# Kernel tuning notes

Measured on AMD Instinct MI355X. Metric: run time of the kernel, lower is better.

Reference implementation:

```python
import jax, jax.numpy as jnp
import numpy as np

EPS = 1e-5
DN = ('NCHW', 'OIHW', 'NCHW')

def conv3(x, w):
    return jax.lax.conv_general_dilated(x, w, (1, 1), 'SAME', dimension_numbers=DN)

def conv1(x, w, b):
    # w: [O, I]
    return jnp.einsum('oi,bihw->bohw', w, x) + b[None, :, None, None]

def bn_relu(x, p):
    # p: [4, C] rows = scale, bias, mean, var (eval-mode BatchNorm2d)
    s, b, m, v = p[0], p[1], p[2], p[3]
    y = s[None, :, None, None] * (x - m[None, :, None, None]) * jax.lax.rsqrt(v[None, :, None, None] + EPS) + b[None, :, None, None]
    return jax.nn.relu(y)

def setup_inputs() -> dict:
    key = jax.random.key(0)
    ks = jax.random.split(key, 24)
    B, Cin, H, W = 2, 2048, 60, 60
    Ci = Cin // 4            # 512 inter_channels
    Cq = Ci // 8             # 64  query/key channels
    Co = 40                  # out_channels (classes)
    f32 = jnp.float32
    def bn(C):
        return jnp.stack([jnp.ones((C,), f32), jnp.zeros((C,), f32), jnp.zeros((C,), f32), jnp.ones((C,), f32)])
    s3 = 1.0 / np.sqrt(9 * Ci)
    inp = {
        'x': jax.random.normal(ks[0], (B, Cin, H, W), f32),
        'd': jax.random.uniform(ks[1], (B, 1, H, W), f32),
        'w_s0': jax.random.normal(ks[2], (Ci, Cin, 3, 3), f32) * (1.0 / np.sqrt(9 * Cin)),
        'bn_s0': bn(Ci),
        'wq': jax.random.normal(ks[3], (Cq, Ci), f32) * (1.0 / np.sqrt(Ci)),
        'bq': jnp.zeros((Cq,), f32),
        'wk': jax.random.normal(ks[4], (Cq, Ci), f32) * (1.0 / np.sqrt(Ci)),
        'bk': jnp.zeros((Cq,), f32),
        'wv': jax.random.normal(ks[5], (Ci, Ci), f32) * (1.0 / np.sqrt(Ci)),
        'bv': jnp.zeros((Ci,), f32),
        'gamma_sa': jnp.zeros((), f32) + 0.5,   # nonzero so attention branch contributes
        'lamb': jnp.zeros((), f32) + 0.3,
        'w_s1': jax.random.normal(ks[6], (Ci, Ci, 3, 3), f32) * s3,
        'bn_s1': bn(Ci),
        'w6': jax.random.normal(ks[7], (Co, Ci), f32) * (1.0 / np.sqrt(Ci)),
        'b6': jnp.zeros((Co,), f32),
        'w_c0': jax.random.normal(ks[8], (Ci, Cin, 3, 3), f32) * (1.0 / np.sqrt(9 * Cin)),
        'bn_c0': bn(Ci),
        'gamma_sc': jnp.zeros((), f32) + 0.5,
        'w_c1': jax.random.normal(ks[9], (Ci, Ci, 3, 3), f32) * s3,
        'bn_c1': bn(Ci),
        'w7': jax.random.normal(ks[10], (Co, Ci), f32) * (1.0 / np.sqrt(Ci)),
        'b7': jnp.zeros((Co,), f32),
        'w8': jax.random.normal(ks[11], (Co, Ci), f32) * (1.0 / np.sqrt(Ci)),
        'b8': jnp.zeros((Co,), f32),
    }
    return inp

def reference(x, d, w_s0, bn_s0, wq, bq, wk, bk, wv, bv, gamma_sa, lamb,
              w_s1, bn_s1, w6, b6, w_c0, bn_c0, gamma_sc, w_c1, bn_c1, w7, b7, w8, b8):
    B, _, H, W = x.shape
    N = H * W
    # ---- position-attention (PAM_Module_Dep, fuse_type='a', depth_order=2) branch ----
    feat1 = bn_relu(conv3(x, w_s0), bn_s0)               # [B, Ci, H, W]
    Ci = feat1.shape[1]
    q = conv1(feat1, wq, bq).reshape(B, -1, N)           # [B, Cq, N]
    k = conv1(feat1, wk, bk).reshape(B, -1, N)           # [B, Cq, N]
    v = conv1(feat1, wv, bv).reshape(B, Ci, N)           # [B, Ci, N]
    energy = jnp.einsum('bcn,bcm->bnm', q, k)            # [B, N, N], n=query pixel
    df = d.reshape(B, N)
    dd = (df[:, :, None] - df[:, None, :]) ** 2          # depth_order == 2
    attention = jax.nn.softmax(energy + lamb * dd, axis=-1)
    sa = jnp.einsum('bcm,bnm->bcn', v, attention).reshape(B, Ci, H, W)
    sa = gamma_sa * sa + feat1
    sa_conv = bn_relu(conv3(sa, w_s1), bn_s1)            # post_conv=True
    sa_output = conv1(sa_conv, w6, b6)                   # Dropout2d is identity in eval
    # ---- channel-attention (CAM_Module) branch ----
    feat2 = bn_relu(conv3(x, w_c0), bn_c0)               # [B, Ci, H, W]
    xf = feat2.reshape(B, Ci, N)
    cen = jnp.einsum('bcn,bdn->bcd', xf, xf)             # [B, Ci, Ci]
    cen = jnp.max(cen, axis=-1, keepdims=True) - cen
    catt = jax.nn.softmax(cen, axis=-1)
    sc = jnp.einsum('bcd,bdn->bcn', catt, xf).reshape(B, Ci, H, W)
    sc = gamma_sc * sc + feat2
    sc_conv = bn_relu(conv3(sc, w_c1), bn_c1)
    sc_output = conv1(sc_conv, w7, b7)
    # ---- fusion head ----
    feat_sum = sa_conv + sc_conv
    sasc_output = conv1(feat_sum, w8, b8)
    return (sasc_output, sa_output, sc_output)
```

## Files before the change

kernel.cpp:

```cpp
#include <hip/hip_runtime.h>
#include <stdint.h>

#define DI __device__ __forceinline__

typedef unsigned short u16;
typedef unsigned int u32;
typedef __attribute__((ext_vector_type(8))) short short8;
typedef __attribute__((ext_vector_type(4))) float floatx4;

constexpr int NPIX = 3600;
constexpr int NK   = 3712;
constexpr int PP   = 4096;
constexpr int GUARD= 128;
constexpr int CIN  = 2048, CI = 512, CQ = 64;

constexpr size_t OFF_XPM    = 0;
constexpr size_t OFF_SAF    = 0;
constexpr size_t OFF_PBUF   = 14745600;
constexpr size_t OFF_SACONV = 0;
constexpr size_t OFF_SCCONV = 8388608;
constexpr size_t R1_END     = 42812416;
constexpr size_t OFF_FEAT1  = R1_END;
constexpr size_t OFF_FEAT2  = OFF_FEAT1 + 8388608;
constexpr size_t OFF_SAPM   = OFF_FEAT2 + 8388608;
constexpr size_t OFF_SCPM   = OFF_SAPM + 8912896;
constexpr size_t OFF_W      = OFF_SCPM + 8912896;
constexpr size_t OFF_WQB = OFF_W;
constexpr size_t OFF_QC  = OFF_W + 655360;
constexpr size_t OFF_KC  = OFF_W + 1576960;
constexpr size_t OFF_VC  = OFF_W + 2498560;
constexpr size_t OFF_WT1 = OFF_W;
constexpr size_t OFF_WT2 = OFF_W + 4718592;
constexpr size_t OFF_VCM = OFF_W + 9871360;
constexpr size_t OFF_CEN = OFF_W + 17473536;
constexpr size_t OFF_CATT= OFF_W + 19570688;
constexpr size_t OFF_WH  = OFF_W + 20619264;
constexpr size_t WS_NEED = OFF_W + 37748736;

DI float b2f(u16 s){ u32 u = ((u32)s)<<16; float f; __builtin_memcpy(&f,&u,4); return f; }
DI u16 f2b(float f){ u32 u; __builtin_memcpy(&u,&f,4); u32 r=(u+0x7fffu+((u>>16)&1u))>>16; return (u16)r; }
DI int pad_of(int n){ int y=n/60, x=n-y*60; return ((y+2)<<6)+x+2; }
DI bool interior(int p){ int py=p>>6, px=p&63; return (py>=2)&&(py<62)&&(px>=2)&&(px<62); }
DI int compact_of(int p){ return ((p>>6)-2)*60 + (p&63) - 2; }
DI void gll16(const void* g, void* l){
  __builtin_amdgcn_global_load_lds((const __attribute__((address_space(1))) void*)g,
                                   (__attribute__((address_space(3))) void*)l, 16, 0, 0);
}
DI float wred_min(float v){
#pragma unroll
  for(int m=32;m;m>>=1) v=fminf(v,__shfl_xor(v,m,64));
  return v;
}
DI float wred_sum(float v){
#pragma unroll
  for(int m=32;m;m>>=1) v+=__shfl_xor(v,m,64);
  return v;
}

struct GArgs {
  const u16 *A, *A2, *B, *B2; u16 *Cb, *Cb2, *Cb3; float* Cf;
  const u16* resid;
  const float *bn, *bn2, *bias, *bias2, *bias3, *gamma, *lambp, *dR, *dC;
  long sA, sB, sC, sres;
  int M, N, KT, ktps, lda, ldb, ldc, Mclamp, Nclamp, nsplit, ksplit, kps;
};

template<int MODE, bool SHIFT, bool NCAT, bool DUALZ, int U, bool SPLITK, bool KCAT2=false>
__global__ __launch_bounds__(256) void k_gemm(GArgs g){
  __shared__ alignas(16) short As[U*4096];
  __shared__ alignas(16) short Bs[U*4096];
  const int bz = blockIdx.z;
  const int sel = DUALZ ? (bz>>1) : 0;
  int bt  = DUALZ ? (bz&1)  : bz;
  int slice = 0;
  if constexpr(SPLITK){ bt = bz / g.ksplit; slice = bz - bt*g.ksplit; }
  const u16* Ab = ((DUALZ && sel) ? g.A2 : g.A) + (long)bt*g.sA;
  const u16* Ab2 = KCAT2 ? (g.A2 + (long)bt*g.sA) : nullptr;
  const u16* Bb = ((DUALZ && sel) ? g.B2 : g.B) + (long)bt*g.sB;
  const int m0 = blockIdx.x*128, n0 = blockIdx.y*128;
  const int tid = threadIdx.x, wid = tid>>6, lane = tid&63;
  const int wr = wid>>1, wc = wid&1;
  const int fr = lane&15, fq = lane>>4;
  const int srow = lane>>2;
  const int swz = ((lane&3) ^ ((lane>>3)&3)) << 3;

  long raB[2], rbB[2];
#pragma unroll
  for(int h=0;h<2;h++){
    long ra = m0 + wid*32 + h*16 + srow;
    if (!SHIFT) ra = (ra > g.Mclamp) ? (long)g.Mclamp : ra;
    raB[h] = ra*(long)g.lda + swz;
    long rb = n0 + wid*32 + h*16 + srow;
    rb = (rb > g.Nclamp) ? (long)g.Nclamp : rb;
    rbB[h] = rb*(long)g.ldb + swz;
  }
  const int ldsOff[2] = { (wid*32)*64, (wid*32+16)*64 };
  const int rswz = (fq ^ ((fr>>1)&3)) << 3;
  const int aRdO = (wr*64+fr)*32 + rswz;
  const int bRdO = (wc*64+fr)*32 + rswz;

  floatx4 acc[4][4];
#pragma unroll
  for(int i=0;i<4;i++)
#pragma unroll
    for(int j=0;j<4;j++)
#pragma unroll
      for(int e=0;e<4;e++) acc[i][j][e]=0.f;

  if constexpr(SHIFT){
    const int KB = g.ktps;
    for(int s=0; s<9; ++s){
      const long aoff = (long)((s/3)*64 + (s-(s/3)*3) - 65)*g.lda;
      const long boff = (long)s*KB*32;
      for(int kb=0; kb<KB; kb+=U){
        __syncthreads();
#pragma unroll
        for(int u=0;u<U;++u){
          const int ko = (kb+u)*32;
#pragma unroll
          for(int h=0;h<2;h++){
            gll16(Ab + raB[h] + aoff + ko, (char*)As + u*8192 + ldsOff[h]);
            gll16(Bb + rbB[h] + boff + ko, (char*)Bs + u*8192 + ldsOff[h]);
          }
        }
        __syncthreads();
#pragma unroll
        for(int u=0;u<U;++u){
          short8 af[4], bfv[4];
#pragma unroll
          for(int mi=0;mi<4;mi++) af[mi]  = *(const short8*)(As + u*4096 + aRdO + mi*512);
#pragma unroll
          for(int ni=0;ni<4;ni++) bfv[ni] = *(const short8*)(Bs + u*4096 + bRdO + ni*512);
#pragma unroll
          for(int mi=0;mi<4;mi++)
#pragma unroll
            for(int ni=0;ni<4;ni++)
              acc[mi][ni] = __builtin_amdgcn_mfma_f32_16x16x32_bf16(af[mi], bfv[ni], acc[mi][ni], 0,0,0);
        }
      }
    }
  } else {
    int kt0 = 0, ktN = g.KT;
    if constexpr(SPLITK){ kt0 = slice*g.kps; ktN = min(g.KT, kt0+g.kps); }
    for(int kt=kt0; kt<ktN; kt+=U){
      __syncthreads();
#pragma unroll
      for(int u=0;u<U;++u){
        if (kt+u < ktN){
          int ko = kt+u;
          const u16* srcA = Ab;
          if constexpr(KCAT2){ if (ko >= (g.KT>>1)){ srcA = Ab2; ko -= (g.KT>>1); } }
          const int koB = (kt+u)*32;
#pragma unroll
          for(int h=0;h<2;h++){
            gll16(srcA + raB[h] + ko*32, (char*)As + u*8192 + ldsOff[h]);
            gll16(Bb + rbB[h] + koB, (char*)Bs + u*8192 + ldsOff[h]);
          }
        }
      }
      __syncthreads();
#pragma unroll
      for(int u=0;u<U;++u){
        if (kt+u < ktN){
          short8 af[4], bfv[4];
#pragma unroll
          for(int mi=0;mi<4;mi++) af[mi]  = *(const short8*)(As + u*4096 + aRdO + mi*512);
#pragma unroll
          for(int ni=0;ni<4;ni++) bfv[ni] = *(const short8*)(Bs + u*4096 + bRdO + ni*512);
#pragma unroll
          for(int mi=0;mi<4;mi++)
#pragma unroll
            for(int ni=0;ni<4;ni++)
              acc[mi][ni] = __builtin_amdgcn_mfma_f32_16x16x32_bf16(af[mi], bfv[ni], acc[mi][ni], 0,0,0);
        }
      }
    }
  }

  float* Cf = (MODE==3) ? g.Cf + (long)bt*g.sC : nullptr;
  const u16* Rb = (MODE==5) ? g.resid + (long)bt*g.sres : nullptr;
  float gamv=0.f;
  if constexpr(MODE==5) gamv = *g.gamma;

#pragma unroll
  for(int ni=0;ni<4;ni++){
    const int gc = n0 + wc*64 + ni*16 + fr;
    if (gc >= g.N) continue;
    if constexpr(MODE==0){
      const float* bnP = g.bn; u16* CbP = g.Cb; int oc = gc;
      if constexpr(DUALZ){ if (sel){ bnP = g.bn2; CbP = g.Cb2; } }
      if constexpr(NCAT){ if (gc >= g.nsplit){ bnP = g.bn2; CbP = g.Cb2; oc = gc - g.nsplit; } }
      CbP += (long)bt*g.sC;
      const float s_=bnP[oc], bb=bnP[CI+oc], mm=bnP[2*CI+oc], vv=bnP[3*CI+oc];
      const float cA = s_*rsqrtf(vv+1e-5f), cB = bb - cA*mm;
#pragma unroll
      for(int mi=0;mi<4;mi++)
#pragma unroll
        for(int j=0;j<4;j++){
          const int gr = m0 + wr*64 + mi*16 + fq*4 + j;
          if (interior(gr)) CbP[(size_t)gr*g.ldc + oc] = f2b(fmaxf(cA*acc[mi][ni][j]+cB, 0.f));
        }
    } else if constexpr(MODE==6){
      u16* dst; int col, ld; float bs;
      if (gc < 64){ dst = g.Cb  + (long)bt*((long)NPIX*CQ); col=gc;     ld=CQ; bs=g.bias[gc]; }
      else if (gc < 128){ dst = g.Cb2 + (long)bt*((long)NPIX*CQ); col=gc-64; ld=CQ; bs=g.bias2[gc-64]; }
      else { dst = g.Cb3 + (long)bt*((long)NPIX*CI); col=gc-128; ld=CI; bs=g.bias3[gc-128]; }
#pragma unroll
      for(int mi=0;mi<4;mi++)
#pragma unroll
        for(int j=0;j<4;j++){
          const int gr = m0 + wr*64 + mi*16 + fq*4 + j;
          if (interior(gr)) dst[(size_t)compact_of(gr)*ld + col] = f2b(acc[mi][ni][j] + bs);
        }
    } else if constexpr(MODE==3){
#pragma unroll
      for(int mi=0;mi<4;mi++)
#pragma unroll
        for(int j=0;j<4;j++){
          const int gr = m0 + wr*64 + mi*16 + fq*4 + j;
          if (gr < g.M){
            if constexpr(SPLITK) atomicAdd(&Cf[(size_t)gr*g.ldc + gc], acc[mi][ni][j]);
            else Cf[(size_t)gr*g.ldc + gc] = acc[mi][ni][j];
          }
        }
    } else if constexpr(MODE==5){
      u16* CbP = g.Cb + (long)bt*g.sC;
#pragma unroll
      for(int mi=0;mi<4;mi++)
#pragma unroll
        for(int j=0;j<4;j++){
          const int gr = m0 + wr*64 + mi*16 + fq*4 + j;
          if (interior(gr)){ const size_t o=(size_t)gr*g.ldc + gc; CbP[o] = f2b(gamv*acc[mi][ni][j] + b2f(Rb[o])); }
        }
    } else if constexpr(MODE==7){
      size_t hb; int oc; const float* bp;
      if (gc < 40){ hb = 0; oc = gc; bp = g.bias; }
      else if (gc < 80){ hb = 288000; oc = gc-40; bp = g.bias2; }
      else { hb = 576000; oc = gc-80; bp = g.bias3; }
      float* dst = g.Cf + hb + (size_t)bt*144000 + (size_t)oc*3600;
      const float bsv = bp[oc];
#pragma unroll
      for(int mi=0;mi<4;mi++)
#pragma unroll
        for(int j=0;j<4;j++){
          const int gr = m0 + wr*64 + mi*16 + fq*4 + j;
          if (interior(gr)) dst[compact_of(gr)] = acc[mi][ni][j] + bsv;
        }
    }
  }
}

__global__ __launch_bounds__(512) void k_esm(const u16* __restrict__ qc, const u16* __restrict__ kc,
    const float* __restrict__ dd, const float* __restrict__ lamp, u16* __restrict__ pb){
  __shared__ float lm[8][16], ll[8][16];
  const int tid = threadIdx.x, wave = tid>>6, lane = tid&63;
  const int fr = lane&15, fq = lane>>4;
  const int q0 = blockIdx.x*16;
  const float lam = *lamp;
  const u16* qp = qc + (size_t)(q0+fr)*CQ + fq*8;
  const short8 qa0 = *(const short8*)(qp);
  const short8 qa1 = *(const short8*)(qp + 32);
  float dr[4];
#pragma unroll
  for(int j=0;j<4;j++) dr[j] = dd[q0 + fq*4 + j];
  float m[4], l[4];
#pragma unroll
  for(int j=0;j<4;j++){ m[j] = -3e38f; l[j] = 0.f; }

  for(int t=wave; t<29; t+=8){
    const int n0 = t*128;
    floatx4 s[8]; float dc[8];
#pragma unroll
    for(int ni=0; ni<8; ++ni){
      const int ccol = min(n0 + ni*16 + fr, NPIX-1);
      const u16* kp = kc + (size_t)ccol*CQ + fq*8;
      const short8 b0 = *(const short8*)(kp);
      const short8 b1 = *(const short8*)(kp + 32);
      floatx4 z = {0.f,0.f,0.f,0.f};
      z = __builtin_amdgcn_mfma_f32_16x16x32_bf16(qa0, b0, z, 0,0,0);
      s[ni] = __builtin_amdgcn_mfma_f32_16x16x32_bf16(qa1, b1, z, 0,0,0);
      dc[ni] = dd[ccol];
    }
#pragma unroll
    for(int j=0;j<4;j++){
      float vals[8]; float tmax = -3e38f;
#pragma unroll
      for(int ni=0;ni<8;ni++){
        const float td = dr[j] - dc[ni];
        float v = s[ni][j] + lam*td*td;
        if (n0 + ni*16 + fr >= NPIX) v = -3e38f;
        vals[ni] = v; tmax = fmaxf(tmax, v);
      }
      tmax = fmaxf(tmax, __shfl_xor(tmax,1,64));
      tmax = fmaxf(tmax, __shfl_xor(tmax,2,64));
      tmax = fmaxf(tmax, __shfl_xor(tmax,4,64));
      tmax = fmaxf(tmax, __shfl_xor(tmax,8,64));
      const float mn = fmaxf(m[j], tmax);
      float ts = 0.f;
#pragma unroll
      for(int ni=0;ni<8;ni++) ts += __expf(vals[ni]-mn);
      ts += __shfl_xor(ts,1,64);
      ts += __shfl_xor(ts,2,64);
      ts += __shfl_xor(ts,4,64);
      ts += __shfl_xor(ts,8,64);
      l[j] = l[j]*__expf(m[j]-mn) + ts;
      m[j] = mn;
    }
  }
  if (fr == 0){
#pragma unroll
    for(int j=0;j<4;j++){ lm[wave][fq*4+j] = m[j]; ll[wave][fq*4+j] = l[j]; }
  }
  __syncthreads();
  float M[4], L[4];
#pragma unroll
  for(int j=0;j<4;j++){
    const int row = fq*4 + j;
    float mm = lm[0][row];
#pragma unroll
    for(int w=1;w<8;w++) mm = fmaxf(mm, lm[w][row]);
    float ss = 0.f;
#pragma unroll
    for(int w=0;w<8;w++) ss += ll[w][row]*__expf(lm[w][row]-mm);
    M[j] = mm; L[j] = 1.f/ss;
  }

  for(int t=wave; t<29; t+=8){
    const int n0 = t*128;
#pragma unroll
    for(int ni=0; ni<8; ++ni){
      const int col = n0 + ni*16 + fr;
      const int ccol = min(col, NPIX-1);
      const u16* kp = kc + (size_t)ccol*CQ + fq*8;
      const short8 b0 = *(const short8*)(kp);
      const short8 b1 = *(const short8*)(kp + 32);
      floatx4 z = {0.f,0.f,0.f,0.f};
      z = __builtin_amdgcn_mfma_f32_16x16x32_bf16(qa0, b0, z, 0,0,0);
      const floatx4 sv = __builtin_amdgcn_mfma_f32_16x16x32_bf16(qa1, b1, z, 0,0,0);
      const float dcv = dd[ccol];
#pragma unroll
      for(int j=0;j<4;j++){
        const int q = q0 + fq*4 + j;
        const float td = dr[j] - dcv;
        float v = sv[j] + lam*td*td;
        if (col >= NPIX) v = -3e38f;
        const float p = __expf(v - M[j])*L[j];
        pb[(size_t)q*NK + col] = f2b(p);
      }
    }
  }
}

__global__ __launch_bounds__(256) void k_zring(u16* __restrict__ base, int C, long slabStride){
  const int row = blockIdx.x, slab = blockIdx.y;
  bool z;
  if (row < GUARD || row >= GUARD+PP) z = true;
  else z = !interior(row - GUARD);
  if (!z) return;
  u16* p = base + (size_t)slab*slabStride + (size_t)row*C;
  for (int i = threadIdx.x*8; i < C; i += 256*8){
    uint4 zz = {0,0,0,0};
    *(uint4*)(p + i) = zz;
  }
}

__global__ __launch_bounds__(256) void k_padx(const float* __restrict__ x, u16* __restrict__ xpm){
  __shared__ alignas(16) u16 t[64][72];
  const int n0 = blockIdx.x*64, c0 = blockIdx.y*64, b = blockIdx.z;
  const float* xb = x + (size_t)b*CIN*NPIX;
  u16* ob = xpm + (size_t)b*(PP+2*GUARD)*CIN + (size_t)GUARD*CIN;
  const int tid = threadIdx.x;
#pragma unroll
  for(int pass=0; pass<2; ++pass){
    const int cl = pass*32 + (tid>>3);
    const int nn = (tid&7)*8;
    const int n = n0 + nn;
    const float* src = xb + (size_t)(c0+cl)*NPIX + n;
    u16 r[8];
    if (n + 7 < NPIX){
      const float4 v0 = *(const float4*)src;
      const float4 v1 = *(const float4*)(src+4);
      r[0]=f2b(v0.x); r[1]=f2b(v0.y); r[2]=f2b(v0.z); r[3]=f2b(v0.w);
      r[4]=f2b(v1.x); r[5]=f2b(v1.y); r[6]=f2b(v1.z); r[7]=f2b(v1.w);
    } else {
#pragma unroll
      for(int j=0;j<8;j++){ const int nj=n+j; r[j] = (nj<NPIX)? f2b(src[j]) : (u16)0; }
    }
    __builtin_memcpy(&t[cl][nn], r, 16);
  }
  __syncthreads();
#pragma unroll
  for(int pass=0; pass<2; ++pass){
    const int nl = pass*32 + (tid>>3);
    const int cc = (tid&7)*8;
    const int n = n0 + nl;
    if (n < NPIX){
      u16 v[8];
#pragma unroll
      for(int j=0;j<8;j++) v[j] = t[cc+j][nl];
      uint4 vv; __builtin_memcpy(&vv, v, 16);
      *(uint4*)(ob + (size_t)pad_of(n)*CIN + c0 + cc) = vv;
    }
  }
}

template<bool PADIN>
__global__ __launch_bounds__(256) void k_to_cm(const u16* __restrict__ in, u16* __restrict__ out,
                                               long sIn, long sOut){
  __shared__ alignas(16) u16 t[64][72];
  const int n0 = blockIdx.x*64, c0 = blockIdx.y*64, b = blockIdx.z;
  const u16* ib = in + (size_t)b*sIn;
  u16* ob = out + (size_t)b*sOut;
  const int tid = threadIdx.x;
#pragma unroll
  for(int pass=0; pass<2; ++pass){
    const int nl = pass*32 + (tid>>3);
    const int cc = (tid&7)*8;
    const int n = n0 + nl;
    uint4 v = {0,0,0,0};
    if (n < NPIX){
      const int r = PADIN ? pad_of(n) : n;
      v = *(const uint4*)(ib + (size_t)r*CI + c0 + cc);
    }
    *(uint4*)&t[nl][cc] = v;
  }
  __syncthreads();
#pragma unroll
  for(int pass=0; pass<2; ++pass){
    const int cl = pass*32 + (tid>>3);
    const int nn = (tid&7)*8;
    const int n = n0 + nn;
    if (n < NK){
      u16 v[8];
#pragma unroll
      for(int j=0;j<8;j++) v[j] = t[nn+j][cl];
      uint4 vv; __builtin_memcpy(&vv, v, 16);
      *(uint4*)(ob + (size_t)(c0+cl)*NK + n) = vv;
    }
  }
}

__global__ __launch_bounds__(256) void k_wt2(const float* __restrict__ wA, const float* __restrict__ wB,
                                             u16* __restrict__ wtA, u16* __restrict__ wtB, int Kc){
  const float* w = blockIdx.y ? wB : wA;
  u16* wt = blockIdx.y ? wtB : wtA;
  const int idx = blockIdx.x*256 + threadIdx.x;
  const int o = idx / Kc, i = idx - o*Kc;
  u16 v[9];
#pragma unroll
  for(int s=0;s<9;s++) v[s] = f2b(w[(size_t)idx*9 + s]);
#pragma unroll
  for(int s=0;s<9;s++) wt[(size_t)o*9*Kc + (size_t)s*Kc + i] = v[s];
}

__global__ __launch_bounds__(256) void k_cvt3(const float* __restrict__ a, int na,
                                              const float* __restrict__ b, int nb,
                                              const float* __restrict__ c, int nc,
                                              u16* __restrict__ dst){
  const int i = blockIdx.x*256 + threadIdx.x;
  float v;
  if (i < na) v = a[i];
  else if (i < na+nb) v = b[i-na];
  else if (i < na+nb+nc) v = c[i-na-nb];
  else return;
  dst[i] = f2b(v);
}

__global__ __launch_bounds__(256) void k_whead(const float* __restrict__ w6, const float* __restrict__ w7,
                                               const float* __restrict__ w8, u16* __restrict__ wh){
  const int idx = blockIdx.x*256 + threadIdx.x;
  const int r = idx >> 10, k = idx & 1023;
  float v = 0.f;
  if (r < 40) v = w8[r*512 + (k & 511)];
  else if (r < 80){ if (k < 512) v = w6[(r-40)*512 + k]; }
  else { if (k >= 512) v = w7[(r-80)*512 + (k-512)]; }
  wh[idx] = f2b(v);
}

__global__ __launch_bounds__(256) void k_csoftmax(const float* __restrict__ cen, u16* __restrict__ catt){
  const int c = blockIdx.x, b = blockIdx.y, tid = threadIdx.x;
  const float* e = cen + ((size_t)b*CI + c)*CI;
  u16* o = catt + ((size_t)b*CI + c)*CI;
  __shared__ float red[8];
  const float a0 = e[tid], a1 = e[tid+256];
  float lmin = fminf(a0,a1);
  lmin = wred_min(lmin);
  if((tid&63)==0) red[tid>>6]=lmin;
  __syncthreads();
  const float m0 = fminf(fminf(red[0],red[1]),fminf(red[2],red[3]));
  const float x0 = __expf(m0-a0), x1 = __expf(m0-a1);
  float ls = x0+x1;
  ls = wred_sum(ls);
  if((tid&63)==0) red[4+(tid>>6)]=ls;
  __syncthreads();
  const float inv = 1.f/(red[4]+red[5]+red[6]+red[7]);
  o[tid] = f2b(x0*inv); o[tid+256] = f2b(x1*inv);
}

__global__ __launch_bounds__(256) void k_pv_ep(const float* __restrict__ saf, const u16* __restrict__ f1,
                                               u16* __restrict__ sapm, const float* __restrict__ gamma){
  const int idx = blockIdx.x*256 + threadIdx.x;
  const int n = idx >> 6, c = (idx & 63) * 8;
  const float gam = *gamma;
  const int p = pad_of(n);
  const float4 v0 = *(const float4*)(saf + (size_t)n*CI + c);
  const float4 v1 = *(const float4*)(saf + (size_t)n*CI + c + 4);
  const uint4 rv = *(const uint4*)(f1 + (size_t)p*CI + c);
  const u16* rp = (const u16*)&rv;
  u16 o[8];
  o[0]=f2b(gam*v0.x + b2f(rp[0])); o[1]=f2b(gam*v0.y + b2f(rp[1]));
  o[2]=f2b(gam*v0.z + b2f(rp[2])); o[3]=f2b(gam*v0.w + b2f(rp[3]));
  o[4]=f2b(gam*v1.x + b2f(rp[4])); o[5]=f2b(gam*v1.y + b2f(rp[5]));
  o[6]=f2b(gam*v1.z + b2f(rp[6])); o[7]=f2b(gam*v1.w + b2f(rp[7]));
  uint4 ov; __builtin_memcpy(&ov, o, 16);
  *(uint4*)(sapm + (size_t)p*CI + c) = ov;
}

extern "C" void kernel_launch(void* const* d_in, const int* in_sizes, int n_in,
                              void* d_out, int out_size, void* d_ws, size_t ws_size,
                              hipStream_t stream){
  (void)in_sizes; (void)n_in; (void)out_size;
  if (ws_size < WS_NEED) return;

  const float* x    = (const float*)d_in[0];
  const float* dd   = (const float*)d_in[1];
  const float* w_s0 = (const float*)d_in[2];
  const float* bn_s0= (const float*)d_in[3];
  const float* wq   = (const float*)d_in[4];
  const float* bq   = (const float*)d_in[5];
  const float* wk   = (const float*)d_in[6];
  const float* bk   = (const float*)d_in[7];
  const float* wv   = (const float*)d_in[8];
  const float* bv   = (const float*)d_in[9];
  const float* gsa  = (const float*)d_in[10];
  const float* lam  = (const float*)d_in[11];
  const float* w_s1 = (const float*)d_in[12];
  const float* bn_s1= (const float*)d_in[13];
  const float* w6   = (const float*)d_in[14];
  const float* b6   = (const float*)d_in[15];
  const float* w_c0 = (const float*)d_in[16];
  const float* bn_c0= (const float*)d_in[17];
  const float* gsc  = (const float*)d_in[18];
  const float* w_c1 = (const float*)d_in[19];
  const float* bn_c1= (const float*)d_in[20];
  const float* w7   = (const float*)d_in[21];
  const float* b7   = (const float*)d_in[22];
  const float* w8   = (const float*)d_in[23];
  const float* b8   = (const float*)d_in[24];

  char* W = (char*)d_ws;
  u16*   XPM   = (u16*)(W + OFF_XPM);
  float* SAF   = (float*)(W + OFF_SAF);
  u16*   PB    = (u16*)(W + OFF_PBUF);
  u16*   SACONV= (u16*)(W + OFF_SACONV);
  u16*   SCCONV= (u16*)(W + OFF_SCCONV);
  u16*   F1    = (u16*)(W + OFF_FEAT1);
  u16*   F2    = (u16*)(W + OFF_FEAT2);
  u16*   SAPM  = (u16*)(W + OFF_SAPM);
  u16*   SCPM  = (u16*)(W + OFF_SCPM);
  u16*   WTT   = (u16*)(W + OFF_W);
  u16*   WQB   = (u16*)(W + OFF_WQB);
  u16*   QC    = (u16*)(W + OFF_QC);
  u16*   KC    = (u16*)(W + OFF_KC);
  u16*   VC    = (u16*)(W + OFF_VC);
  u16*   WT1   = (u16*)(W + OFF_WT1);
  u16*   WT2   = (u16*)(W + OFF_WT2);
  u16*   WH    = (u16*)(W + OFF_WH);
  u16*   VCM   = (u16*)(W + OFF_VCM);
  u16*   F2CM  = VCM;
  float* CEN   = (float*)(W + OFF_CEN);
  u16*   CATT  = (u16*)(W + OFF_CATT);
  float* OUT   = (float*)d_out;

  k_zring<<<dim3(PP+2*GUARD, 2),256,0,stream>>>(XPM,  CIN, (long)(PP+2*GUARD)*CIN);
  k_zring<<<dim3(PP+2*GUARD, 4),256,0,stream>>>(SAPM, CI,  (long)(PP+2*GUARD)*CI);

  k_padx<<<dim3(57,32,2),256,0,stream>>>(x, XPM);

  k_wt2<<<dim3((512*2048)/256, 2),256,0,stream>>>(w_s0, w_c0, WTT, WTT + (size_t)512*9*2048, 2048);
  GArgs a{};
  a.A = XPM + (size_t)GUARD*CIN; a.B = WTT; a.Cb = F1; a.Cb2 = F2;
  a.bn = bn_s0; a.bn2 = bn_c0;
  a.sA = (long)(PP+2*GUARD)*CIN; a.sB = 0; a.sC = (long)PP*CI;
  a.M = PP; a.N = 1024; a.nsplit = 512; a.KT = 576; a.ktps = 64;
  a.lda = CIN; a.ldb = 9*2048; a.ldc = CI; a.Mclamp = PP-1; a.Nclamp = 1023;
  k_gemm<0,true,true,false,4,false><<<dim3(32,8,2),256,0,stream>>>(a);

  k_cvt3<<<dim3((64*512+64*512+512*512)/256),256,0,stream>>>(wq, 64*512, wk, 64*512, wv, 512*512, WQB);

  GArgs q{};
  q.A = F1; q.sA = (long)PP*CI; q.lda = CI;
  q.M = PP; q.Mclamp = PP-1; q.KT = 16; q.ktps = 16;
  q.B = WQB; q.sB = 0; q.ldb = CI; q.N = 640; q.Nclamp = 639;
  q.Cb = QC; q.Cb2 = KC; q.Cb3 = VC; q.bias = bq; q.bias2 = bk; q.bias3 = bv;
  k_gemm<6,false,false,false,4,false><<<dim3(32,5,2),256,0,stream>>>(q);

  k_to_cm<false><<<dim3(NK/64, CI/64, 2),256,0,stream>>>(VC, VCM, (long)NPIX*CI, (long)CI*NK);

  for(int bb=0; bb<2; ++bb){
    k_esm<<<dim3(225),512,0,stream>>>(QC + (size_t)bb*NPIX*CQ, KC + (size_t)bb*NPIX*CQ,
                                      dd + (size_t)bb*NPIX, lam, PB);
    hipMemsetAsync(SAF, 0, (size_t)NPIX*CI*4, stream);
    GArgs p{};
    p.A = PB; p.B = VCM + (size_t)bb*CI*NK;
    p.Cf = SAF;
    p.M = NPIX; p.N = CI; p.KT = NK/32; p.ktps = NK/32;
    p.lda = NK; p.ldb = NK; p.ldc = CI; p.sC = 0;
    p.Mclamp = NPIX-1; p.Nclamp = CI-1;
    p.ksplit = 4; p.kps = NK/128;
    k_gemm<3,false,false,false,4,true><<<dim3(29, 4, 4),256,0,stream>>>(p);
    k_pv_ep<<<dim3(NPIX*CI/8/256),256,0,stream>>>(SAF, F1 + (size_t)bb*PP*CI,
                                                  SAPM + (size_t)bb*(PP+2*GUARD)*CI + (size_t)GUARD*CI, gsa);
  }

  k_to_cm<true><<<dim3(NK/64, CI/64, 2),256,0,stream>>>(F2, F2CM, (long)PP*CI, (long)CI*NK);
  hipMemsetAsync(CEN, 0, (size_t)2*CI*CI*4, stream);
  GArgs c{};
  c.A = F2CM; c.B = F2CM; c.Cf = CEN;
  c.sA = (long)CI*NK; c.sB = (long)CI*NK; c.sC = (long)CI*CI;
  c.M = CI; c.N = CI; c.KT = NK/32; c.ktps = NK/32;
  c.lda = NK; c.ldb = NK; c.ldc = CI; c.Mclamp = CI-1; c.Nclamp = CI-1;
  c.ksplit = 8; c.kps = (NK/32 + 7)/8;
  k_gemm<3,false,false,false,1,true><<<dim3(4, 4, 16),256,0,stream>>>(c);
  k_csoftmax<<<dim3(CI,2),256,0,stream>>>(CEN, CATT);
  GArgs s{};
  s.A = F2; s.B = CATT;
  s.Cb = SCPM + (size_t)GUARD*CI;
  s.resid = F2; s.gamma = gsc;
  s.sA = (long)PP*CI; s.sB = (long)CI*CI; s.sC = (long)(PP+2*GUARD)*CI; s.sres = (long)PP*CI;
  s.M = PP; s.N = CI; s.KT = 16; s.ktps = 16;
  s.lda = CI; s.ldb = CI; s.ldc = CI; s.Mclamp = PP-1; s.Nclamp = CI-1;
  k_gemm<5,false,false,false,4,false><<<dim3(32, 4, 2),256,0,stream>>>(s);

  k_wt2<<<dim3((512*512)/256, 2),256,0,stream>>>(w_s1, w_c1, WT1, WT2, 512);
  k_whead<<<dim3(120*1024/256),256,0,stream>>>(w6, w7, w8, WH);
  GArgs t{};
  t.A = SAPM + (size_t)GUARD*CI; t.A2 = SCPM + (size_t)GUARD*CI;
  t.B = WT1; t.B2 = WT2;
  t.Cb = SACONV; t.Cb2 = SCCONV; t.bn = bn_s1; t.bn2 = bn_c1;
  t.sA = (long)(PP+2*GUARD)*CI; t.sB = 0; t.sC = (long)PP*CI;
  t.M = PP; t.N = CI; t.KT = 144; t.ktps = 16;
  t.lda = CI; t.ldb = 9*512; t.ldc = CI; t.Mclamp = PP-1; t.Nclamp = CI-1;
  k_gemm<0,true,false,true,4,false><<<dim3(32,4,4),256,0,stream>>>(t);

  GArgs h{};
  h.A = SACONV; h.A2 = SCCONV; h.B = WH; h.Cf = OUT;
  h.bias = b8; h.bias2 = b6; h.bias3 = b7;
  h.sA = (long)PP*CI; h.sB = 0; h.sC = 0;
  h.M = PP; h.N = 120; h.KT = 32; h.ktps = 32;
  h.lda = CI; h.ldb = 1024; h.ldc = 0; h.Mclamp = PP-1; h.Nclamp = 119;
  k_gemm<7,false,false,false,4,false,true><<<dim3(32,1,2),256,0,stream>>>(h);
}
```

Baseline: 740.6 us.

## Split-K first 3x3 conv per batch, cache ESM scores, stage probability writes via LDS

New measurement: 867.5 us. 1.17x slower.

```diff
diff --git a/kernel.cpp b/kernel.cpp
--- a/kernel.cpp
+++ b/kernel.cpp
@@ -62,7 +62,7 @@
   const u16* resid;
   const float *bn, *bn2, *bias, *bias2, *bias3, *gamma, *lambp, *dR, *dC;
   long sA, sB, sC, sres;
-  int M, N, KT, ktps, lda, ldb, ldc, Mclamp, Nclamp, nsplit, ksplit, kps;
+  int M, N, KT, ktps, lda, ldb, ldc, Mclamp, Nclamp, nsplit, ksplit, kps, kblog;
 };
 
 template<int MODE, bool SHIFT, bool NCAT, bool DUALZ, int U, bool SPLITK, bool KCAT2=false>
@@ -107,7 +107,45 @@
 #pragma unroll
       for(int e=0;e<4;e++) acc[i][j][e]=0.f;
 
-  if constexpr(SHIFT){
+  if constexpr(SHIFT && SPLITK){
+    const int KBm1 = g.ktps - 1;
+    const int kt0 = slice*g.kps;
+    const int ktN = min(g.KT, kt0 + g.kps);
+    for(int kt=kt0; kt<ktN; kt+=U){
+      __syncthreads();
+#pragma unroll
+      for(int u=0;u<U;++u){
+        const int gu = kt+u;
+        if (gu < ktN){
+          const int s_ = gu >> g.kblog;
+          const int s3 = s_/3;
+          const long aoff = (long)(s3*64 + (s_-s3*3) - 65)*g.lda + ((long)(gu & KBm1)<<5);
+          const long boff = (long)gu<<5;
+#pragma unroll
+          for(int h=0;h<2;h++){
+            gll16(Ab + raB[h] + aoff, (char*)As + u*8192 + ldsOff[h]);
+            gll16(Bb + rbB[h] + boff, (char*)Bs + u*8192 + ldsOff[h]);
+          }
+        }
+      }
+      __syncthreads();
+#pragma unroll
+      for(int u=0;u<U;++u){
+        if (kt+u < ktN){
+          short8 af[4], bfv[4];
+#pragma unroll
+          for(int mi=0;mi<4;mi++) af[mi]  = *(const short8*)(As + u*4096 + aRdO + mi*512);
+#pragma unroll
+          for(int ni=0;ni<4;ni++) bfv[ni] = *(const short8*)(Bs + u*4096 + bRdO + ni*512);
+#pragma unroll
+          for(int mi=0;mi<4;mi++)
+#pragma unroll
+            for(int ni=0;ni<4;ni++)
+              acc[mi][ni] = __builtin_amdgcn_mfma_f32_16x16x32_bf16(af[mi], bfv[ni], acc[mi][ni], 0,0,0);
+        }
+      }
+    }
+  } else if constexpr(SHIFT){
     const int KB = g.ktps;
     for(int s=0; s<9; ++s){
       const long aoff = (long)((s/3)*64 + (s-(s/3)*3) - 65)*g.lda;
@@ -250,9 +288,35 @@
   }
 }
 
+__global__ __launch_bounds__(256) void k_bnrelu(const float* __restrict__ cacc,
+    const float* __restrict__ bn1, const float* __restrict__ bn2,
+    u16* __restrict__ f1, u16* __restrict__ f2){
+  const int idx = blockIdx.x*256 + threadIdx.x;
+  const int n = idx >> 7, c = (idx & 127) * 8;
+  const int p = pad_of(n);
+  const float4 v0 = *(const float4*)(cacc + (size_t)p*1024 + c);
+  const float4 v1 = *(const float4*)(cacc + (size_t)p*1024 + c + 4);
+  const bool second = c >= 512;
+  const float* bn = second ? bn2 : bn1;
+  u16* f = second ? f2 : f1;
+  const int oc = c & 511;
+  const float vv[8] = {v0.x,v0.y,v0.z,v0.w,v1.x,v1.y,v1.z,v1.w};
+  u16 o[8];
+#pragma unroll
+  for(int j=0;j<8;j++){
+    const int ocj = oc + j;
+    const float s = bn[ocj], b = bn[CI+ocj], m = bn[2*CI+ocj], var = bn[3*CI+ocj];
+    const float cA = s*rsqrtf(var+1e-5f);
+    o[j] = f2b(fmaxf(cA*(vv[j]-m)+b, 0.f));
+  }
+  uint4 ov; __builtin_memcpy(&ov, o, 16);
+  *(uint4*)(f + (size_t)p*CI + oc) = ov;
+}
+
 __global__ __launch_bounds__(512) void k_esm(const u16* __restrict__ qc, const u16* __restrict__ kc,
     const float* __restrict__ dd, const float* __restrict__ lamp, u16* __restrict__ pb){
   __shared__ float lm[8][16], ll[8][16];
+  __shared__ alignas(16) u16 pemit[8][16][128];
   const int tid = threadIdx.x, wave = tid>>6, lane = tid&63;
   const int fr = lane&15, fq = lane>>4;
   const int q0 = blockIdx.x*16;
@@ -266,45 +330,50 @@
   float m[4], l[4];
 #pragma unroll
   for(int j=0;j<4;j++){ m[j] = -3e38f; l[j] = 0.f; }
-
-  for(int t=wave; t<29; t+=8){
-    const int n0 = t*128;
-    floatx4 s[8]; float dc[8];
-#pragma unroll
-    for(int ni=0; ni<8; ++ni){
-      const int ccol = min(n0 + ni*16 + fr, NPIX-1);
-      const u16* kp = kc + (size_t)ccol*CQ + fq*8;
-      const short8 b0 = *(const short8*)(kp);
-      const short8 b1 = *(const short8*)(kp + 32);
-      floatx4 z = {0.f,0.f,0.f,0.f};
-      z = __builtin_amdgcn_mfma_f32_16x16x32_bf16(qa0, b0, z, 0,0,0);
-      s[ni] = __builtin_amdgcn_mfma_f32_16x16x32_bf16(qa1, b1, z, 0,0,0);
-      dc[ni] = dd[ccol];
-    }
-#pragma unroll
-    for(int j=0;j<4;j++){
-      float vals[8]; float tmax = -3e38f;
-#pragma unroll
-      for(int ni=0;ni<8;ni++){
-        const float td = dr[j] - dc[ni];
-        float v = s[ni][j] + lam*td*td;
-        if (n0 + ni*16 + fr >= NPIX) v = -3e38f;
-        vals[ni] = v; tmax = fmaxf(tmax, v);
+  float vals[4][8][4];
+
+#pragma unroll
+  for(int tt=0; tt<4; ++tt){
+    const int t = wave + tt*8;
+    if (t < 29){
+      const int n0 = t*128;
+      floatx4 s[8]; float dc[8];
+#pragma unroll
+      for(int ni=0; ni<8; ++ni){
+        const int ccol = min(n0 + ni*16 + fr, NPIX-1);
+        const u16* kp = kc + (size_t)ccol*CQ + fq*8;
+        const short8 b0 = *(const short8*)(kp);
+        const short8 b1 = *(const short8*)(kp + 32);
+        floatx4 z = {0.f,0.f,0.f,0.f};
+        z = __builtin_amdgcn_mfma_f32_16x16x32_bf16(qa0, b0, z, 0,0,0);
+        s[ni] = __builtin_amdgcn_mfma_f32_16x16x32_bf16(qa1, b1, z, 0,0,0);
+        dc[ni] = dd[ccol];
       }
-      tmax = fmaxf(tmax, __shfl_xor(tmax,1,64));
-      tmax = fmaxf(tmax, __shfl_xor(tmax,2,64));
-      tmax = fmaxf(tmax, __shfl_xor(tmax,4,64));
-      tmax = fmaxf(tmax, __shfl_xor(tmax,8,64));
-      const float mn = fmaxf(m[j], tmax);
-      float ts = 0.f;
-#pragma unroll
-      for(int ni=0;ni<8;ni++) ts += __expf(vals[ni]-mn);
-      ts += __shfl_xor(ts,1,64);
-      ts += __shfl_xor(ts,2,64);
-      ts += __shfl_xor(ts,4,64);
-      ts += __shfl_xor(ts,8,64);
-      l[j] = l[j]*__expf(m[j]-mn) + ts;
-      m[j] = mn;
+#pragma unroll
+      for(int j=0;j<4;j++){
+        float tmax = -3e38f;
+#pragma unroll
+        for(int ni=0;ni<8;ni++){
+          const float td = dr[j] - dc[ni];
+          float v = s[ni][j] + lam*td*td;
+          if (n0 + ni*16 + fr >= NPIX) v = -3e38f;
+          vals[tt][ni][j] = v; tmax = fmaxf(tmax, v);
+        }
+        tmax = fmaxf(tmax, __shfl_xor(tmax,1,64));
+        tmax = fmaxf(tmax, __shfl_xor(tmax,2,64));
+        tmax = fmaxf(tmax, __shfl_xor(tmax,4,64));
+        tmax = fmaxf(tmax, __shfl_xor(tmax,8,64));
+        const float mn = fmaxf(m[j], tmax);
+        float ts = 0.f;
+#pragma unroll
+        for(int ni=0;ni<8;ni++) ts += __expf(vals[tt][ni][j]-mn);
+        ts += __shfl_xor(ts,1,64);
+        ts += __shfl_xor(ts,2,64);
+        ts += __shfl_xor(ts,4,64);
+        ts += __shfl_xor(ts,8,64);
+        l[j] = l[j]*__expf(m[j]-mn) + ts;
+        m[j] = mn;
+      }
     }
   }
   if (fr == 0){
@@ -325,27 +394,23 @@
     M[j] = mm; L[j] = 1.f/ss;
   }
 
-  for(int t=wave; t<29; t+=8){
-    const int n0 = t*128;
-#pragma unroll
-    for(int ni=0; ni<8; ++ni){
-      const int col = n0 + ni*16 + fr;
-      const int ccol = min(col, NPIX-1);
-      const u16* kp = kc + (size_t)ccol*CQ + fq*8;
-      const short8 b0 = *(const short8*)(kp);
-      const short8 b1 = *(const short8*)(kp + 32);
-      floatx4 z = {0.f,0.f,0.f,0.f};
-      z = __builtin_amdgcn_mfma_f32_16x16x32_bf16(qa0, b0, z, 0,0,0);
-      const floatx4 sv = __builtin_amdgcn_mfma_f32_16x16x32_bf16(qa1, b1, z, 0,0,0);
-      const float dcv = dd[ccol];
-#pragma unroll
-      for(int j=0;j<4;j++){
-        const int q = q0 + fq*4 + j;
-        const float td = dr[j] - dcv;
-        float v = sv[j] + lam*td*td;
-        if (col >= NPIX) v = -3e38f;
-        const float p = __expf(v - M[j])*L[j];
-        pb[(size_t)q*NK + col] = f2b(p);
+#pragma unroll
+  for(int tt=0; tt<4; ++tt){
+    const int t = wave + tt*8;
+    if (t < 29){
+      const int n0 = t*128;
+#pragma unroll
+      for(int ni=0;ni<8;ni++)
+#pragma unroll
+        for(int j=0;j<4;j++)
+          pemit[wave][fq*4+j][ni*16+fr] = f2b(__expf(vals[tt][ni][j] - M[j])*L[j]);
+      asm volatile("s_waitcnt lgkmcnt(0)" ::: "memory");
+#pragma unroll
+      for(int it=0; it<4; ++it){
+        const int row = it*4 + fq;
+        const int c8 = fr*8;
+        uint4 v; __builtin_memcpy(&v, &pemit[wave][row][c8], 16);
+        *(uint4*)(pb + (size_t)(q0+row)*NK + n0 + c8) = v;
       }
     }
   }
@@ -558,6 +623,7 @@
   u16*   F2    = (u16*)(W + OFF_FEAT2);
   u16*   SAPM  = (u16*)(W + OFF_SAPM);
   u16*   SCPM  = (u16*)(W + OFF_SCPM);
+  float* CACC  = (float*)(W + OFF_SAPM);
   u16*   WTT   = (u16*)(W + OFF_W);
   u16*   WQB   = (u16*)(W + OFF_WQB);
   u16*   QC    = (u16*)(W + OFF_QC);
@@ -573,18 +639,24 @@
   float* OUT   = (float*)d_out;
 
   k_zring<<<dim3(PP+2*GUARD, 2),256,0,stream>>>(XPM,  CIN, (long)(PP+2*GUARD)*CIN);
-  k_zring<<<dim3(PP+2*GUARD, 4),256,0,stream>>>(SAPM, CI,  (long)(PP+2*GUARD)*CI);
 
   k_padx<<<dim3(57,32,2),256,0,stream>>>(x, XPM);
 
   k_wt2<<<dim3((512*2048)/256, 2),256,0,stream>>>(w_s0, w_c0, WTT, WTT + (size_t)512*9*2048, 2048);
-  GArgs a{};
-  a.A = XPM + (size_t)GUARD*CIN; a.B = WTT; a.Cb = F1; a.Cb2 = F2;
-  a.bn = bn_s0; a.bn2 = bn_c0;
-  a.sA = (long)(PP+2*GUARD)*CIN; a.sB = 0; a.sC = (long)PP*CI;
-  a.M = PP; a.N = 1024; a.nsplit = 512; a.KT = 576; a.ktps = 64;
-  a.lda = CIN; a.ldb = 9*2048; a.ldc = CI; a.Mclamp = PP-1; a.Nclamp = 1023;
-  k_gemm<0,true,true,false,4,false><<<dim3(32,8,2),256,0,stream>>>(a);
+  for(int bb=0; bb<2; ++bb){
+    hipMemsetAsync(CACC, 0, (size_t)PP*1024*4, stream);
+    GArgs a{};
+    a.A = XPM + (size_t)bb*(PP+2*GUARD)*CIN + (size_t)GUARD*CIN;
+    a.B = WTT; a.Cf = CACC;
+    a.sA = 0; a.sB = 0; a.sC = 0;
+    a.M = PP; a.N = 1024; a.KT = 576; a.ktps = 64; a.kblog = 6;
+    a.lda = CIN; a.ldb = 9*2048; a.ldc = 1024; a.Mclamp = PP-1; a.Nclamp = 1023;
+    a.ksplit = 4; a.kps = 144;
+    k_gemm<3,true,false,false,2,true><<<dim3(32,8,4),256,0,stream>>>(a);
+    k_bnrelu<<<dim3(460800/256),256,0,stream>>>(CACC, bn_s0, bn_c0,
+        F1 + (size_t)bb*PP*CI, F2 + (size_t)bb*PP*CI);
+  }
+  k_zring<<<dim3(PP+2*GUARD, 4),256,0,stream>>>(SAPM, CI, (long)(PP+2*GUARD)*CI);
 
   k_cvt3<<<dim3((64*512+64*512+512*512)/256),256,0,stream>>>(wq, 64*512, wk, 64*512, wv, 512*512, WQB);
 
@@ -621,7 +693,7 @@
   c.M = CI; c.N = CI; c.KT = NK/32; c.ktps = NK/32;
   c.lda = NK; c.ldb = NK; c.ldc = CI; c.Mclamp = CI-1; c.Nclamp = CI-1;
   c.ksplit = 8; c.kps = (NK/32 + 7)/8;
-  k_gemm<3,false,false,false,1,true><<<dim3(4, 4, 16),256,0,stream>>>(c);
+  k_gemm<3,false,false,false,4,true><<<dim3(4, 4, 16),256,0,stream>>>(c);
   k_csoftmax<<<dim3(CI,2),256,0,stream>>>(CEN, CATT);
   GArgs s{};
   s.A = F2; s.B = CATT;
```

## Cache attention logits in registers and stage P writes through LDS

Applied to the files above, without the earlier changes.

After: 727.3 us. Within noise of the previous version (-1.8%).

```diff
diff --git a/kernel.cpp b/kernel.cpp
--- a/kernel.cpp
+++ b/kernel.cpp
@@ -253,6 +253,7 @@
 __global__ __launch_bounds__(512) void k_esm(const u16* __restrict__ qc, const u16* __restrict__ kc,
     const float* __restrict__ dd, const float* __restrict__ lamp, u16* __restrict__ pb){
   __shared__ float lm[8][16], ll[8][16];
+  __shared__ alignas(16) u16 pemit[8][16][128];
   const int tid = threadIdx.x, wave = tid>>6, lane = tid&63;
   const int fr = lane&15, fq = lane>>4;
   const int q0 = blockIdx.x*16;
@@ -266,45 +267,50 @@
   float m[4], l[4];
 #pragma unroll
   for(int j=0;j<4;j++){ m[j] = -3e38f; l[j] = 0.f; }
-
-  for(int t=wave; t<29; t+=8){
-    const int n0 = t*128;
-    floatx4 s[8]; float dc[8];
-#pragma unroll
-    for(int ni=0; ni<8; ++ni){
-      const int ccol = min(n0 + ni*16 + fr, NPIX-1);
-      const u16* kp = kc + (size_t)ccol*CQ + fq*8;
-      const short8 b0 = *(const short8*)(kp);
-      const short8 b1 = *(const short8*)(kp + 32);
-      floatx4 z = {0.f,0.f,0.f,0.f};
-      z = __builtin_amdgcn_mfma_f32_16x16x32_bf16(qa0, b0, z, 0,0,0);
-      s[ni] = __builtin_amdgcn_mfma_f32_16x16x32_bf16(qa1, b1, z, 0,0,0);
-      dc[ni] = dd[ccol];
-    }
-#pragma unroll
-    for(int j=0;j<4;j++){
-      float vals[8]; float tmax = -3e38f;
-#pragma unroll
-      for(int ni=0;ni<8;ni++){
-        const float td = dr[j] - dc[ni];
-        float v = s[ni][j] + lam*td*td;
-        if (n0 + ni*16 + fr >= NPIX) v = -3e38f;
-        vals[ni] = v; tmax = fmaxf(tmax, v);
+  float vals[4][8][4];
+
+#pragma unroll
+  for(int tt=0; tt<4; ++tt){
+    const int t = wave + tt*8;
+    if (t < 29){
+      const int n0 = t*128;
+      floatx4 s[8]; float dc[8];
+#pragma unroll
+      for(int ni=0; ni<8; ++ni){
+        const int ccol = min(n0 + ni*16 + fr, NPIX-1);
+        const u16* kp = kc + (size_t)ccol*CQ + fq*8;
+        const short8 b0 = *(const short8*)(kp);
+        const short8 b1 = *(const short8*)(kp + 32);
+        floatx4 z = {0.f,0.f,0.f,0.f};
+        z = __builtin_amdgcn_mfma_f32_16x16x32_bf16(qa0, b0, z, 0,0,0);
+        s[ni] = __builtin_amdgcn_mfma_f32_16x16x32_bf16(qa1, b1, z, 0,0,0);
+        dc[ni] = dd[ccol];
       }
-      tmax = fmaxf(tmax, __shfl_xor(tmax,1,64));
-      tmax = fmaxf(tmax, __shfl_xor(tmax,2,64));
-      tmax = fmaxf(tmax, __shfl_xor(tmax,4,64));
-      tmax = fmaxf(tmax, __shfl_xor(tmax,8,64));
-      const float mn = fmaxf(m[j], tmax);
-      float ts = 0.f;
-#pragma unroll
-      for(int ni=0;ni<8;ni++) ts += __expf(vals[ni]-mn);
-      ts += __shfl_xor(ts,1,64);
-      ts += __shfl_xor(ts,2,64);
-      ts += __shfl_xor(ts,4,64);
-      ts += __shfl_xor(ts,8,64);
-      l[j] = l[j]*__expf(m[j]-mn) + ts;
-      m[j] = mn;
+#pragma unroll
+      for(int j=0;j<4;j++){
+        float tmax = -3e38f;
+#pragma unroll
+        for(int ni=0;ni<8;ni++){
+          const float td = dr[j] - dc[ni];
+          float v = s[ni][j] + lam*td*td;
+          if (n0 + ni*16 + fr >= NPIX) v = -3e38f;
+          vals[tt][ni][j] = v; tmax = fmaxf(tmax, v);
+        }
+        tmax = fmaxf(tmax, __shfl_xor(tmax,1,64));
+        tmax = fmaxf(tmax, __shfl_xor(tmax,2,64));
+        tmax = fmaxf(tmax, __shfl_xor(tmax,4,64));
+        tmax = fmaxf(tmax, __shfl_xor(tmax,8,64));
+        const float mn = fmaxf(m[j], tmax);
+        float ts = 0.f;
+#pragma unroll
+        for(int ni=0;ni<8;ni++) ts += __expf(vals[tt][ni][j]-mn);
+        ts += __shfl_xor(ts,1,64);
+        ts += __shfl_xor(ts,2,64);
+        ts += __shfl_xor(ts,4,64);
+        ts += __shfl_xor(ts,8,64);
+        l[j] = l[j]*__expf(m[j]-mn) + ts;
+        m[j] = mn;
+      }
     }
   }
   if (fr == 0){
@@ -325,27 +331,23 @@
     M[j] = mm; L[j] = 1.f/ss;
   }
 
-  for(int t=wave; t<29; t+=8){
-    const int n0 = t*128;
-#pragma unroll
-    for(int ni=0; ni<8; ++ni){
-      const int col = n0 + ni*16 + fr;
-      const int ccol = min(col, NPIX-1);
-      const u16* kp = kc + (size_t)ccol*CQ + fq*8;
-      const short8 b0 = *(const short8*)(kp);
-      const short8 b1 = *(const short8*)(kp + 32);
-      floatx4 z = {0.f,0.f,0.f,0.f};
-      z = __builtin_amdgcn_mfma_f32_16x16x32_bf16(qa0, b0, z, 0,0,0);
-      const floatx4 sv = __builtin_amdgcn_mfma_f32_16x16x32_bf16(qa1, b1, z, 0,0,0);
-      const float dcv = dd[ccol];
-#pragma unroll
-      for(int j=0;j<4;j++){
-        const int q = q0 + fq*4 + j;
-        const float td = dr[j] - dcv;
-        float v = sv[j] + lam*td*td;
-        if (col >= NPIX) v = -3e38f;
-        const float p = __expf(v - M[j])*L[j];
-        pb[(size_t)q*NK + col] = f2b(p);
+#pragma unroll
+  for(int tt=0; tt<4; ++tt){
+    const int t = wave + tt*8;
+    if (t < 29){
+      const int n0 = t*128;
+#pragma unroll
+      for(int ni=0;ni<8;ni++)
+#pragma unroll
+        for(int j=0;j<4;j++)
+          pemit[wave][fq*4+j][ni*16+fr] = f2b(__expf(vals[tt][ni][j] - M[j])*L[j]);
+      asm volatile("s_waitcnt lgkmcnt(0)" ::: "memory");
+#pragma unroll
+      for(int it=0; it<4; ++it){
+        const int row = it*4 + fq;
+        const int c8 = fr*8;
+        uint4 v; __builtin_memcpy(&v, &pemit[wave][row][c8], 16);
+        *(uint4*)(pb + (size_t)(q0+row)*NK + n0 + c8) = v;
       }
     }
   }
@@ -621,7 +623,7 @@
   c.M = CI; c.N = CI; c.KT = NK/32; c.ktps = NK/32;
   c.lda = NK; c.ldb = NK; c.ldc = CI; c.Mclamp = CI-1; c.Nclamp = CI-1;
   c.ksplit = 8; c.kps = (NK/32 + 7)/8;
-  k_gemm<3,false,false,false,1,true><<<dim3(4, 4, 16),256,0,stream>>>(c);
+  k_gemm<3,false,false,false,4,true><<<dim3(4, 4, 16),256,0,stream>>>(c);
   k_csoftmax<<<dim3(CI,2),256,0,stream>>>(CEN, CATT);
   GArgs s{};
   s.A = F2; s.B = CATT;
```
